# Kernel tuning notes

Measured on AMD Instinct MI355X. Metric: run time of the kernel, lower is better.

## Reference

```python
import jax, jax.numpy as jnp
import numpy as np
from jax import lax


def setup_inputs() -> dict:
    key = jax.random.key(0)
    k0, k1, k2 = jax.random.split(key, 3)
    B, D, L, K = 8, 4096, 4096, 4
    x = jax.random.randint(k0, (B, D, L), -128, 128, dtype=jnp.int32).astype(jnp.int8)
    weight = jax.random.randint(k1, (D, K), -128, 128, dtype=jnp.int32).astype(jnp.int8)
    bias = jax.random.randint(k2, (D,), -128, 128, dtype=jnp.int32).astype(jnp.int8)
    return {
        "x": x,
        "weight": weight,
        "bias": bias,
        "input_scale": jnp.array([0.05], jnp.float32),
        "weight_scale": jnp.array([0.01], jnp.float32),
        "output_scale": jnp.array([0.04], jnp.float32),
        "bias_scale": jnp.array([0.02], jnp.float32),
    }


def reference(x, weight, bias, input_scale, weight_scale, output_scale, bias_scale):
    """int8 depthwise causal conv1d with fused dequant -> conv -> bias -> silu -> requant.

    x:      (B, D, L) int8 activations
    weight: (D, K)    int8 depthwise taps
    bias:   (D,)      int8 bias
    Returns (B, D, L) int8 requantized output.
    """
    D, K = weight.shape
    # Dequantize
    xf = x.astype(jnp.float32) * input_scale[0]                       # (B, D, L)
    wf = weight.astype(jnp.float32) * weight_scale[0]                  # (D, K)
    bf = bias.astype(jnp.float32) * bias_scale[0]                      # (D,)
    # Causal depthwise conv: pad K-1 on the left, groups == D
    y = lax.conv_general_dilated(
        xf, wf[:, None, :],                                            # (D, 1, K) OIH
        window_strides=(1,), padding=[(K - 1, 0)],
        dimension_numbers=("NCH", "OIH", "NCH"),
        feature_group_count=D,
    )
    y = jax.nn.silu(y + bf[None, :, None])
    # Requantize to int8
    yq = jnp.clip(jnp.round(y / output_scale[0]), -128, 127).astype(jnp.int8)
    return yq
```

## Files before the change

### kernel.cpp

```cpp
#include <hip/hip_runtime.h>


#define Dq 4096
#define Lq 4096
#define VPR (Lq / 4)

__global__ void __launch_bounds__(256)
qconv1d_kernel(const int* __restrict__ x,
               const int* __restrict__ w,
               const int* __restrict__ bias,
               const float* __restrict__ s_in,
               const float* __restrict__ s_w,
               const float* __restrict__ s_out,
               const float* __restrict__ s_b,
               int* __restrict__ out,
               int nvec) {
    const float sc      = s_in[0] * s_w[0];
    const float inv_out = 1.0f / s_out[0];
    const float sb      = s_b[0];

    const int4* __restrict__ xv = (const int4*)x;
    const int4* __restrict__ wv = (const int4*)w;
    int4* __restrict__ ov = (int4*)out;

    int idx    = blockIdx.x * blockDim.x + threadIdx.x;
    int stride = gridDim.x * blockDim.x;

    for (; idx < nvec; idx += stride) {
        const int v   = idx & (VPR - 1);
        const int row = idx >> 10;
        const int d   = row & (Dq - 1);

        int4 cur = xv[idx];
        int4 prev;
        if (v == 0) {
            prev = make_int4(0, 0, 0, 0);
        } else {
            prev = xv[idx - 1];
        }
        const int4 wt = wv[d];
        const float bf = (float)bias[d] * sb;

        int xs[8] = {prev.x, prev.y, prev.z, prev.w, cur.x, cur.y, cur.z, cur.w};

        int4 o;
        int* op = &o.x;
        #pragma unroll
        for (int j = 0; j < 4; ++j) {
            int s = xs[j + 1] * wt.x + xs[j + 2] * wt.y
                  + xs[j + 3] * wt.z + xs[j + 4] * wt.w;
            float y = (float)s * sc + bf;
            float sig = 1.0f / (1.0f + __expf(-y));
            float sil = y * sig;
            float q = rintf(sil * inv_out);
            q = fminf(fmaxf(q, -128.0f), 127.0f);
            op[j] = (int)q;
        }
        ov[idx] = o;
    }
}

extern "C" void kernel_launch(void* const* d_in, const int* in_sizes, int n_in,
                              void* d_out, int out_size, void* d_ws, size_t ws_size,
                              hipStream_t stream) {
    const int*   x    = (const int*)d_in[0];
    const int*   w    = (const int*)d_in[1];
    const int*   bias = (const int*)d_in[2];
    const float* s_in = (const float*)d_in[3];
    const float* s_w  = (const float*)d_in[4];
    const float* s_out= (const float*)d_in[5];
    const float* s_b  = (const float*)d_in[6];
    int* out = (int*)d_out;

    const int nvec = out_size / 4;
    const int block = 256;
    int grid = 8192;
    if (grid > (nvec + block - 1) / block) grid = (nvec + block - 1) / block;

    qconv1d_kernel<<<grid, block, 0, stream>>>(x, w, bias, s_in, s_w, s_out, s_b,
                                               out, nvec);
}
```

Before: 214.0 us.

## Map one block per row with four vectors per thread and nontemporal stores

```diff
diff --git a/kernel.cpp b/kernel.cpp
--- a/kernel.cpp
+++ b/kernel.cpp
@@ -2,8 +2,9 @@
 
 
 #define Dq 4096
-#define Lq 4096
-#define VPR (Lq / 4)
+#define VPR 1024
+
+typedef int int4v __attribute__((ext_vector_type(4)));
 
 __global__ void __launch_bounds__(256)
 qconv1d_kernel(const int* __restrict__ x,
@@ -13,51 +14,57 @@
                const float* __restrict__ s_w,
                const float* __restrict__ s_out,
                const float* __restrict__ s_b,
-               int* __restrict__ out,
-               int nvec) {
+               int* __restrict__ out) {
+    const int row  = blockIdx.x;
+    const int d    = row & (Dq - 1);
+    const int t    = threadIdx.x;
+    const long base = (long)row * VPR;
+
+    const int4v* __restrict__ xv = (const int4v*)x;
+    const int4v* __restrict__ wv = (const int4v*)w;
+    int4v* __restrict__ ov = (int4v*)out;
+
+    int4v cur0 = xv[base + 0 * 256 + t];
+    int4v cur1 = xv[base + 1 * 256 + t];
+    int4v cur2 = xv[base + 2 * 256 + t];
+    int4v cur3 = xv[base + 3 * 256 + t];
+    int4v zero = {0, 0, 0, 0};
+    int4v prev0 = (t == 0) ? zero : xv[base + 0 * 256 + t - 1];
+    int4v prev1 = xv[base + 1 * 256 + t - 1];
+    int4v prev2 = xv[base + 2 * 256 + t - 1];
+    int4v prev3 = xv[base + 3 * 256 + t - 1];
+
+    const int4v wt = wv[d];
     const float sc      = s_in[0] * s_w[0];
     const float inv_out = 1.0f / s_out[0];
-    const float sb      = s_b[0];
+    const float bf      = (float)bias[d] * s_b[0];
 
-    const int4* __restrict__ xv = (const int4*)x;
-    const int4* __restrict__ wv = (const int4*)w;
-    int4* __restrict__ ov = (int4*)out;
-
-    int idx    = blockIdx.x * blockDim.x + threadIdx.x;
-    int stride = gridDim.x * blockDim.x;
-
-    for (; idx < nvec; idx += stride) {
-        const int v   = idx & (VPR - 1);
-        const int row = idx >> 10;
-        const int d   = row & (Dq - 1);
-
-        int4 cur = xv[idx];
-        int4 prev;
-        if (v == 0) {
-            prev = make_int4(0, 0, 0, 0);
-        } else {
-            prev = xv[idx - 1];
-        }
-        const int4 wt = wv[d];
-        const float bf = (float)bias[d] * sb;
-
-        int xs[8] = {prev.x, prev.y, prev.z, prev.w, cur.x, cur.y, cur.z, cur.w};
-
-        int4 o;
-        int* op = &o.x;
+    int4v o0, o1, o2, o3;
+    #pragma unroll
+    for (int g = 0; g < 4; ++g) {
+        int4v cur  = (g == 0) ? cur0  : (g == 1) ? cur1  : (g == 2) ? cur2  : cur3;
+        int4v prev = (g == 0) ? prev0 : (g == 1) ? prev1 : (g == 2) ? prev2 : prev3;
+        int xs[8] = {prev[0], prev[1], prev[2], prev[3],
+                     cur[0],  cur[1],  cur[2],  cur[3]};
+        int4v o;
         #pragma unroll
         for (int j = 0; j < 4; ++j) {
-            int s = xs[j + 1] * wt.x + xs[j + 2] * wt.y
-                  + xs[j + 3] * wt.z + xs[j + 4] * wt.w;
+            int s = xs[j + 1] * wt[0] + xs[j + 2] * wt[1]
+                  + xs[j + 3] * wt[2] + xs[j + 4] * wt[3];
             float y = (float)s * sc + bf;
             float sig = 1.0f / (1.0f + __expf(-y));
             float sil = y * sig;
             float q = rintf(sil * inv_out);
             q = fminf(fmaxf(q, -128.0f), 127.0f);
-            op[j] = (int)q;
+            o[j] = (int)q;
         }
-        ov[idx] = o;
+        if (g == 0) o0 = o; else if (g == 1) o1 = o; else if (g == 2) o2 = o; else o3 = o;
     }
+
+    __builtin_nontemporal_store(o0, &ov[base + 0 * 256 + t]);
+    __builtin_nontemporal_store(o1, &ov[base + 1 * 256 + t]);
+    __builtin_nontemporal_store(o2, &ov[base + 2 * 256 + t]);
+    __builtin_nontemporal_store(o3, &ov[base + 3 * 256 + t]);
 }
 
 extern "C" void kernel_launch(void* const* d_in, const int* in_sizes, int n_in,
@@ -72,11 +79,6 @@
     const float* s_b  = (const float*)d_in[6];
     int* out = (int*)d_out;
 
-    const int nvec = out_size / 4;
-    const int block = 256;
-    int grid = 8192;
-    if (grid > (nvec + block - 1) / block) grid = (nvec + block - 1) / block;
-
-    qconv1d_kernel<<<grid, block, 0, stream>>>(x, w, bias, s_in, s_w, s_out, s_b,
-                                               out, nvec);
+    const int rows = out_size / (VPR * 4);
+    qconv1d_kernel<<<rows, 256, 0, stream>>>(x, w, bias, s_in, s_w, s_out, s_b, out);
 }
```

New measurement: 181.4 us, median of 2. -15.3%, faster.
